# Performance work log

Hardware: AMD Instinct MI355X
Metric: run time of the kernel (lower is better)

Reference implementation:

```python
import jax, jax.numpy as jnp
import numpy as np

B, DIM, HID, K, G, MID = 1024, 384, 64, 8, 48, 128
EPS = 1e-06


def _gaussian_8x8():
    t = jnp.arange(K, dtype=jnp.float32) - 3.5
    g = jnp.exp(-(t[:, None] ** 2 + t[None, :] ** 2) / (2.0 * 2.0 ** 2))
    return g / g.sum()


def setup_inputs() -> dict:
    key = jax.random.key(0)
    ks = jax.random.split(key, 16)
    inp = {
        "x": jax.random.normal(ks[0], (B, DIM), dtype=jnp.float32),
        "W": jax.random.normal(ks[1], (DIM, HID), dtype=jnp.float32) * 0.02,
        "b": jax.random.normal(ks[2], (DIM, HID), dtype=jnp.float32) * 0.02,
        "patch_weight": _gaussian_8x8(),  # learnable 8x8, softmaxed in forward
        "pair_w1": jax.random.normal(ks[3], (G, G), dtype=jnp.float32) * 0.02,
        "pair_b1": jax.random.normal(ks[4], (G, G), dtype=jnp.float32) * 0.02,
        "pair_w2": jax.random.normal(ks[5], (G, G), dtype=jnp.float32) * 0.02,
        "pair_b2": jax.random.normal(ks[6], (G, G), dtype=jnp.float32) * 0.02,
        # nn.Linear(G, DIM)
        "proj_w": jax.random.normal(ks[7], (DIM, G), dtype=jnp.float32) * (1.0 / np.sqrt(G)),
        "proj_b": jax.random.normal(ks[8], (DIM,), dtype=jnp.float32) * 0.02,
        # nn.Linear(HID, MID)
        "down_w": jax.random.normal(ks[9], (MID, HID), dtype=jnp.float32) * (1.0 / np.sqrt(HID)),
        "down_b": jax.random.normal(ks[10], (MID,), dtype=jnp.float32) * 0.02,
        # nn.Linear(MID, HID)
        "up_w": jax.random.normal(ks[11], (HID, MID), dtype=jnp.float32) * (1.0 / np.sqrt(MID)),
        "up_b": jax.random.normal(ks[12], (HID,), dtype=jnp.float32) * 0.02,
    }
    return inp


def _leaky(v):
    return jnp.where(v >= 0, v, 0.01 * v)


def reference(x, W, b, patch_weight, pair_w1, pair_b1, pair_w2, pair_b2,
              proj_w, proj_b, down_w, down_b, up_w, up_b):
    # scale / inverse-bias GELU features: (B, DIM, HID)
    s = x[:, :, None]
    inv = 1.0 / (jnp.abs(s) + EPS)
    H = jax.nn.gelu(s * W[None] + inv * b[None], approximate=False)
    # Gram matrix over hidden dim: (B, DIM, DIM)
    P = jnp.einsum('bik,bjk->bij', H, H)
    # learnable gaussian patch pooling (softmax over flattened 8x8 weights)
    w = jax.nn.softmax(patch_weight.reshape(-1)).reshape(K, K)
    Pg = jnp.einsum('bgkhl,kl->bgh', P.reshape(-1, G, K, G, K), w)  # (B, G, G)
    # two elementwise gated leaky layers
    Pg = _leaky(Pg * pair_w1[None] + pair_b1[None])
    Pg = _leaky(Pg * pair_w2[None] + pair_b2[None])
    # softmax + nonlinear row reduction -> (B, G)
    row_soft = jax.nn.softmax(Pg, axis=-1)
    row_weights = (1.0 / (1.0 + row_soft ** 2)).sum(axis=-1)
    # project 48 -> 384, scale rows of H
    scales = row_weights @ proj_w.T + proj_b  # (B, DIM)
    H = H * scales[:, :, None]
    # tiny MLP on hidden dim
    z = _leaky(H @ down_w.T + down_b)
    z = _leaky(z @ up_w.T + up_b)
    return z
```

## Files before the change

### kernel.cpp

```cpp
#include <hip/hip_runtime.h>


#define EPSF 1e-6f

typedef __attribute__((ext_vector_type(8))) short bf16x8;
typedef __attribute__((ext_vector_type(4))) float f32x4;
typedef __attribute__((ext_vector_type(4))) unsigned short u16x4;

__device__ __forceinline__ unsigned short f2bf(float f) {
    union { float f; unsigned int u; } v; v.f = f;
    unsigned int r = v.u + 0x7fffu + ((v.u >> 16) & 1u);
    return (unsigned short)(r >> 16);
}
__device__ __forceinline__ float bf2f(unsigned short h) {
    union { unsigned int u; float f; } v; v.u = ((unsigned int)h) << 16;
    return v.f;
}
__device__ __forceinline__ float leaky(float v) { return v >= 0.0f ? v : 0.01f * v; }
__device__ __forceinline__ int key8(int r) { return (r ^ (r >> 3)) & 7; }
__device__ __forceinline__ float gelu_f(float u) {
    float t  = 0.7978845608028654f * (u + 0.044715f * u * u * u);
    float e  = __expf(2.0f * t);
    float th = 1.0f - 2.0f / (e + 1.0f);
    return 0.5f * u * (1.0f + th);
}

__global__ void prep(const float* __restrict__ proj_w,
                     const float* __restrict__ down_w,
                     const float* __restrict__ up_w,
                     float* __restrict__ ws) {
    int idx = blockIdx.x * blockDim.x + threadIdx.x;
    unsigned short* wb = (unsigned short*)(ws + 18432);
    if (idx < 18432) {
        int i = idx / 48, g = idx % 48;
        ws[g * 384 + i] = proj_w[idx];
    } else if (idx < 26624) {
        int k = idx - 18432;
        wb[k] = f2bf(down_w[k]);
    } else if (idx < 34816) {
        int k = idx - 26624;
        wb[8192 + k] = f2bf(up_w[k]);
    }
}

__global__ __launch_bounds__(512, 2) void fused_main(
    const float* __restrict__ x,
    const float* __restrict__ W,
    const float* __restrict__ bb,
    const float* __restrict__ patch_weight,
    const float* __restrict__ pw1, const float* __restrict__ pb1,
    const float* __restrict__ pw2, const float* __restrict__ pb2,
    const float* __restrict__ proj_b,
    const float* __restrict__ down_b,
    const float* __restrict__ up_b,
    const float* __restrict__ ws,
    float* __restrict__ out)
{
    __shared__ __align__(16) unsigned short sH[24576];
    __shared__ __align__(16) unsigned short sM[24576];
    __shared__ __align__(16) unsigned short sZ1[16384];
    __shared__ float sPg[48 * 49];
    __shared__ float sw[64];
    __shared__ float srw[48];
    __shared__ float sScale[384];
    __shared__ float sDb[128];
    __shared__ float sUb[64];

    const int t = threadIdx.x;
    const int b = blockIdx.x;
    const int wv = t >> 6, lane = t & 63, q = lane >> 4, r = lane & 15;
    const float* projT = ws;
    const unsigned short* dwB = (const unsigned short*)(ws + 18432);
    const unsigned short* uwB = dwB + 8192;
    unsigned short* sDW = sM;
    unsigned short* sUW = sM + 8192;

    if (t < 64) {
        float p = patch_weight[t];
        float m = p;
        for (int o = 32; o > 0; o >>= 1) m = fmaxf(m, __shfl_xor(m, o));
        float e = __expf(p - m);
        float s = e;
        for (int o = 32; o > 0; o >>= 1) s += __shfl_xor(s, o);
        sw[t] = e / s;
    }

    for (int j = 0; j < 12; ++j) {
        int idx4 = j * 512 + t;
        int base = idx4 * 4;
        int i = base >> 6, c0 = base & 63;
        float4 w4 = ((const float4*)W)[idx4];
        float4 b4 = ((const float4*)bb)[idx4];
        float xi  = x[b * 384 + i];
        float inv = 1.0f / (fabsf(xi) + EPSF);
        u16x4 hv;
        hv[0] = f2bf(gelu_f(xi * w4.x + inv * b4.x));
        hv[1] = f2bf(gelu_f(xi * w4.y + inv * b4.y));
        hv[2] = f2bf(gelu_f(xi * w4.z + inv * b4.z));
        hv[3] = f2bf(gelu_f(xi * w4.w + inv * b4.w));
        int cb = c0 >> 3, cc = c0 & 7;
        *(u16x4*)&sH[i * 64 + (cb ^ key8(i)) * 8 + cc] = hv;
    }
    __syncthreads();

    for (int jj = 0; jj < 6; ++jj) {
        int n = jj * 512 + t;
        int g = n >> 6, rem = n & 63, l = rem >> 3, cb = rem & 7;
        float acc[8];
        #pragma unroll
        for (int z = 0; z < 8; ++z) acc[z] = 0.0f;
        #pragma unroll
        for (int k = 0; k < 8; ++k) {
            int i = g * 8 + k;
            bf16x8 hv = *(const bf16x8*)&sH[i * 64 + (cb ^ key8(i)) * 8];
            float wk = sw[k * 8 + l];
            #pragma unroll
            for (int z = 0; z < 8; ++z) acc[z] += wk * bf2f((unsigned short)hv[z]);
        }
        int cbg = l * 8 + cb;
        int cbs = (cbg & ~7) | ((cbg ^ key8(g)) & 7);
        bf16x8 mv;
        #pragma unroll
        for (int z = 0; z < 8; ++z) mv[z] = (short)f2bf(acc[z]);
        *(bf16x8*)&sM[g * 512 + cbs * 8] = mv;
    }
    __syncthreads();

    for (int tt = wv; tt < 9; tt += 8) {
        int tg = tt / 3, th = tt % 3;
        f32x4 acc = {0.f, 0.f, 0.f, 0.f};
        for (int ks = 0; ks < 16; ++ks) {
            int kf = ks * 32 + q * 8;
            int g = tg * 16 + r;
            int cbg = kf >> 3;
            int cbs = (cbg & ~7) | ((cbg ^ key8(g)) & 7);
            bf16x8 av = *(const bf16x8*)&sM[g * 512 + cbs * 8];
            int h = th * 16 + r;
            int i = h * 8 + (kf >> 6);
            int cbh = (kf & 63) >> 3;
            bf16x8 bv = *(const bf16x8*)&sH[i * 64 + (cbh ^ key8(i)) * 8];
            acc = __builtin_amdgcn_mfma_f32_16x16x32_bf16(av, bv, acc, 0, 0, 0);
        }
        #pragma unroll
        for (int reg = 0; reg < 4; ++reg) {
            int g = tg * 16 + q * 4 + reg;
            int h = th * 16 + r;
            int idx = g * 48 + h;
            float v = acc[reg];
            v = leaky(v * pw1[idx] + pb1[idx]);
            v = leaky(v * pw2[idx] + pb2[idx]);
            sPg[g * 49 + h] = v;
        }
    }
    __syncthreads();

    if (t < 48) {
        const float* row = &sPg[t * 49];
        float mx = row[0];
        for (int h = 1; h < 48; ++h) mx = fmaxf(mx, row[h]);
        float s = 0.0f;
        for (int h = 0; h < 48; ++h) s += __expf(row[h] - mx);
        float invs = 1.0f / s;
        float rw = 0.0f;
        for (int h = 0; h < 48; ++h) {
            float p = __expf(row[h] - mx) * invs;
            rw += 1.0f / (1.0f + p * p);
        }
        srw[t] = rw;
    } else if (t >= 64) {
        for (int cid = t - 64; cid < 2048; cid += 448) {
            if (cid < 1024) {
                int nrow = cid >> 3, cb = cid & 7;
                bf16x8 v = *(const bf16x8*)&dwB[cid * 8];
                *(bf16x8*)&sDW[nrow * 64 + (cb ^ key8(nrow)) * 8] = v;
            } else {
                int c2 = cid - 1024;
                int rrow = c2 >> 4, cb = c2 & 15;
                bf16x8 v = *(const bf16x8*)&uwB[c2 * 8];
                int cbs = (cb & 8) | ((cb ^ key8(rrow)) & 7);
                *(bf16x8*)&sUW[rrow * 128 + cbs * 8] = v;
            }
        }
    }
    if (t >= 64 && t < 192)  sDb[t - 64]  = down_b[t - 64];
    if (t >= 192 && t < 256) sUb[t - 192] = up_b[t - 192];
    __syncthreads();

    if (t < 384) {
        float s = proj_b[t];
        for (int g = 0; g < 48; ++g) s += srw[g] * projT[g * 384 + t];
        sScale[t] = s;
    }
    __syncthreads();

    for (int rt = 0; rt < 3; ++rt) {
        {
            const int mt = wv;
            f32x4 acc[8];
            #pragma unroll
            for (int nt = 0; nt < 8; ++nt) acc[nt] = (f32x4){0.f, 0.f, 0.f, 0.f};
            #pragma unroll
            for (int ks = 0; ks < 2; ++ks) {
                int i = rt * 128 + mt * 16 + r;
                int cb = ks * 4 + q;
                bf16x8 av = *(const bf16x8*)&sH[i * 64 + (cb ^ key8(i)) * 8];
                #pragma unroll
                for (int nt = 0; nt < 8; ++nt) {
                    int nrow = nt * 16 + r;
                    bf16x8 bv = *(const bf16x8*)&sDW[nrow * 64 + (cb ^ key8(nrow)) * 8];
                    acc[nt] = __builtin_amdgcn_mfma_f32_16x16x32_bf16(av, bv, acc[nt], 0, 0, 0);
                }
            }
            #pragma unroll
            for (int nt = 0; nt < 8; ++nt) {
                #pragma unroll
                for (int reg = 0; reg < 4; ++reg) {
                    int rl = mt * 16 + q * 4 + reg;
                    int i = rt * 128 + rl;
                    int mm = nt * 16 + r;
                    float v = leaky(acc[nt][reg] * sScale[i] + sDb[mm]);
                    int cb = mm >> 3;
                    int cbs = (cb & 8) | ((cb ^ key8(rl)) & 7);
                    sZ1[rl * 128 + cbs * 8 + (mm & 7)] = f2bf(v);
                }
            }
        }
        __syncthreads();
        {
            const int mt = wv;
            f32x4 acc2[4];
            #pragma unroll
            for (int nt = 0; nt < 4; ++nt) acc2[nt] = (f32x4){0.f, 0.f, 0.f, 0.f};
            #pragma unroll
            for (int ks = 0; ks < 4; ++ks) {
                int rl = mt * 16 + r;
                int cb = ks * 4 + q;
                int cbs = (cb & 8) | ((cb ^ key8(rl)) & 7);
                bf16x8 av = *(const bf16x8*)&sZ1[rl * 128 + cbs * 8];
                #pragma unroll
                for (int nt = 0; nt < 4; ++nt) {
                    int nrow = nt * 16 + r;
                    int cbs2 = (cb & 8) | ((cb ^ key8(nrow)) & 7);
                    bf16x8 bv = *(const bf16x8*)&sUW[nrow * 128 + cbs2 * 8];
                    acc2[nt] = __builtin_amdgcn_mfma_f32_16x16x32_bf16(av, bv, acc2[nt], 0, 0, 0);
                }
            }
            #pragma unroll
            for (int nt = 0; nt < 4; ++nt) {
                #pragma unroll
                for (int reg = 0; reg < 4; ++reg) {
                    int i = rt * 128 + mt * 16 + q * 4 + reg;
                    int cp = nt * 16 + r;
                    float v = leaky(acc2[nt][reg] + sUb[cp]);
                    out[(b * 384 + i) * 64 + cp] = v;
                }
            }
        }
        __syncthreads();
    }
}

extern "C" void kernel_launch(void* const* d_in, const int* in_sizes, int n_in,
                              void* d_out, int out_size, void* d_ws, size_t ws_size,
                              hipStream_t stream) {
    const float* x      = (const float*)d_in[0];
    const float* W      = (const float*)d_in[1];
    const float* bb     = (const float*)d_in[2];
    const float* pw     = (const float*)d_in[3];
    const float* pw1    = (const float*)d_in[4];
    const float* pb1    = (const float*)d_in[5];
    const float* pw2    = (const float*)d_in[6];
    const float* pb2    = (const float*)d_in[7];
    const float* proj_w = (const float*)d_in[8];
    const float* proj_b = (const float*)d_in[9];
    const float* down_w = (const float*)d_in[10];
    const float* down_b = (const float*)d_in[11];
    const float* up_w   = (const float*)d_in[12];
    const float* up_b   = (const float*)d_in[13];
    float* out = (float*)d_out;
    float* ws  = (float*)d_ws;

    prep<<<(34816 + 255) / 256, 256, 0, stream>>>(proj_w, down_w, up_w, ws);
    fused_main<<<1024, 512, 0, stream>>>(x, W, bb, pw, pw1, pb1, pw2, pb2,
                                         proj_b, down_b, up_b, ws, out);
}
```

Before: 220.0 us.

## Use 1024-thread blocks, reshape MLP tiling, warp-parallel softmax, cheaper GELU math

Doubles the block size to 1024 threads and reworks every stage to match. Pooling now lets each thread produce four patch columns, and the per-row softmax becomes a wavefront shuffle reduction instead of a 48-thread serial loop. The MLP tiles change to 2 passes of 192 rows with a 4x4 wave grid, and shared buffers are aliased to fit. GELU, reciprocal and leaky are rewritten with rcp, fma and fmax. The intent is to cut serial phases and instruction count, at the cost of register pressure under __launch_bounds__(1024,4) and a larger LDS footprint that may limit occupancy.

Result: faster. 197.6 us (-10.2%).

```diff
diff --git a/kernel.cpp b/kernel.cpp
--- a/kernel.cpp
+++ b/kernel.cpp
@@ -16,13 +16,13 @@
     union { unsigned int u; float f; } v; v.u = ((unsigned int)h) << 16;
     return v.f;
 }
-__device__ __forceinline__ float leaky(float v) { return v >= 0.0f ? v : 0.01f * v; }
+__device__ __forceinline__ float leaky(float v) { return fmaxf(v, 0.01f * v); }
 __device__ __forceinline__ int key8(int r) { return (r ^ (r >> 3)) & 7; }
 __device__ __forceinline__ float gelu_f(float u) {
-    float t  = 0.7978845608028654f * (u + 0.044715f * u * u * u);
-    float e  = __expf(2.0f * t);
-    float th = 1.0f - 2.0f / (e + 1.0f);
-    return 0.5f * u * (1.0f + th);
+    float t = u * (1.5957691216f + 0.0713548163f * (u * u));
+    float e = __expf(t);
+    float r = __builtin_amdgcn_rcpf(e + 1.0f);
+    return fmaf(-u, r, u);
 }
 
 __global__ void prep(const float* __restrict__ proj_w,
@@ -43,7 +43,7 @@
     }
 }
 
-__global__ __launch_bounds__(512, 2) void fused_main(
+__global__ __launch_bounds__(1024, 4) void fused_main(
     const float* __restrict__ x,
     const float* __restrict__ W,
     const float* __restrict__ bb,
@@ -57,9 +57,8 @@
     float* __restrict__ out)
 {
     __shared__ __align__(16) unsigned short sH[24576];
-    __shared__ __align__(16) unsigned short sM[24576];
-    __shared__ __align__(16) unsigned short sZ1[16384];
-    __shared__ float sPg[48 * 49];
+    __shared__ __align__(16) unsigned short sRB[24576];
+    __shared__ __align__(16) unsigned short sZ1[24576];
     __shared__ float sw[64];
     __shared__ float srw[48];
     __shared__ float sScale[384];
@@ -72,8 +71,10 @@
     const float* projT = ws;
     const unsigned short* dwB = (const unsigned short*)(ws + 18432);
     const unsigned short* uwB = dwB + 8192;
-    unsigned short* sDW = sM;
-    unsigned short* sUW = sM + 8192;
+    unsigned short* sM  = sRB;
+    unsigned short* sDW = sRB;
+    unsigned short* sUW = sRB + 8192;
+    float* sPg = (float*)(sRB + 16384);
 
     if (t < 64) {
         float p = patch_weight[t];
@@ -82,177 +83,208 @@
         float e = __expf(p - m);
         float s = e;
         for (int o = 32; o > 0; o >>= 1) s += __shfl_xor(s, o);
-        sw[t] = e / s;
-    }
-
-    for (int j = 0; j < 12; ++j) {
-        int idx4 = j * 512 + t;
+        sw[t] = e * __builtin_amdgcn_rcpf(s);
+    }
+
+    for (int j = 0; j < 6; ++j) {
+        int idx4 = j * 1024 + t;
         int base = idx4 * 4;
         int i = base >> 6, c0 = base & 63;
         float4 w4 = ((const float4*)W)[idx4];
         float4 b4 = ((const float4*)bb)[idx4];
         float xi  = x[b * 384 + i];
-        float inv = 1.0f / (fabsf(xi) + EPSF);
+        float inv = __builtin_amdgcn_rcpf(fabsf(xi) + EPSF);
         u16x4 hv;
-        hv[0] = f2bf(gelu_f(xi * w4.x + inv * b4.x));
-        hv[1] = f2bf(gelu_f(xi * w4.y + inv * b4.y));
-        hv[2] = f2bf(gelu_f(xi * w4.z + inv * b4.z));
-        hv[3] = f2bf(gelu_f(xi * w4.w + inv * b4.w));
+        hv[0] = f2bf(gelu_f(fmaf(xi, w4.x, inv * b4.x)));
+        hv[1] = f2bf(gelu_f(fmaf(xi, w4.y, inv * b4.y)));
+        hv[2] = f2bf(gelu_f(fmaf(xi, w4.z, inv * b4.z)));
+        hv[3] = f2bf(gelu_f(fmaf(xi, w4.w, inv * b4.w)));
         int cb = c0 >> 3, cc = c0 & 7;
-        *(u16x4*)&sH[i * 64 + (cb ^ key8(i)) * 8 + cc] = hv;
-    }
-    __syncthreads();
-
-    for (int jj = 0; jj < 6; ++jj) {
-        int n = jj * 512 + t;
-        int g = n >> 6, rem = n & 63, l = rem >> 3, cb = rem & 7;
-        float acc[8];
-        #pragma unroll
-        for (int z = 0; z < 8; ++z) acc[z] = 0.0f;
+        *(u16x4*)&sH[i * 64 + ((cb ^ key8(i)) << 3) + cc] = hv;
+    }
+    __syncthreads();
+
+    if (t < 768) {
+        const int cb = t & 7, lq = (t >> 3) & 1, g = t >> 4;
+        float acc[4][8];
+        #pragma unroll
+        for (int a = 0; a < 4; ++a)
+            #pragma unroll
+            for (int cc = 0; cc < 8; ++cc) acc[a][cc] = 0.0f;
         #pragma unroll
         for (int k = 0; k < 8; ++k) {
             int i = g * 8 + k;
-            bf16x8 hv = *(const bf16x8*)&sH[i * 64 + (cb ^ key8(i)) * 8];
-            float wk = sw[k * 8 + l];
-            #pragma unroll
-            for (int z = 0; z < 8; ++z) acc[z] += wk * bf2f((unsigned short)hv[z]);
-        }
-        int cbg = l * 8 + cb;
-        int cbs = (cbg & ~7) | ((cbg ^ key8(g)) & 7);
-        bf16x8 mv;
-        #pragma unroll
-        for (int z = 0; z < 8; ++z) mv[z] = (short)f2bf(acc[z]);
-        *(bf16x8*)&sM[g * 512 + cbs * 8] = mv;
-    }
-    __syncthreads();
-
-    for (int tt = wv; tt < 9; tt += 8) {
-        int tg = tt / 3, th = tt % 3;
-        f32x4 acc = {0.f, 0.f, 0.f, 0.f};
+            bf16x8 hv = *(const bf16x8*)&sH[i * 64 + ((cb ^ key8(i)) << 3)];
+            f32x4 w4 = *(const f32x4*)&sw[k * 8 + lq * 4];
+            float hf[8];
+            #pragma unroll
+            for (int cc = 0; cc < 8; ++cc) hf[cc] = bf2f((unsigned short)hv[cc]);
+            #pragma unroll
+            for (int a = 0; a < 4; ++a)
+                #pragma unroll
+                for (int cc = 0; cc < 8; ++cc) acc[a][cc] = fmaf(w4[a], hf[cc], acc[a][cc]);
+        }
+        #pragma unroll
+        for (int a = 0; a < 4; ++a) {
+            int l = lq * 4 + a;
+            bf16x8 mv;
+            #pragma unroll
+            for (int cc = 0; cc < 8; ++cc) mv[cc] = (short)f2bf(acc[a][cc]);
+            *(bf16x8*)&sM[g * 512 + ((l * 8 + (cb ^ key8(g))) << 3)] = mv;
+        }
+    }
+    __syncthreads();
+
+    f32x4 pacc = {0.f, 0.f, 0.f, 0.f};
+    if (wv < 9) {
+        const int tg = wv / 3, th = wv % 3;
         for (int ks = 0; ks < 16; ++ks) {
             int kf = ks * 32 + q * 8;
             int g = tg * 16 + r;
             int cbg = kf >> 3;
             int cbs = (cbg & ~7) | ((cbg ^ key8(g)) & 7);
-            bf16x8 av = *(const bf16x8*)&sM[g * 512 + cbs * 8];
+            bf16x8 av = *(const bf16x8*)&sM[g * 512 + (cbs << 3)];
             int h = th * 16 + r;
             int i = h * 8 + (kf >> 6);
             int cbh = (kf & 63) >> 3;
-            bf16x8 bv = *(const bf16x8*)&sH[i * 64 + (cbh ^ key8(i)) * 8];
-            acc = __builtin_amdgcn_mfma_f32_16x16x32_bf16(av, bv, acc, 0, 0, 0);
+            bf16x8 bv = *(const bf16x8*)&sH[i * 64 + ((cbh ^ key8(i)) << 3)];
+            pacc = __builtin_amdgcn_mfma_f32_16x16x32_bf16(av, bv, pacc, 0, 0, 0);
         }
         #pragma unroll
         for (int reg = 0; reg < 4; ++reg) {
             int g = tg * 16 + q * 4 + reg;
             int h = th * 16 + r;
             int idx = g * 48 + h;
-            float v = acc[reg];
-            v = leaky(v * pw1[idx] + pb1[idx]);
-            v = leaky(v * pw2[idx] + pb2[idx]);
-            sPg[g * 49 + h] = v;
-        }
-    }
-    __syncthreads();
-
-    if (t < 48) {
-        const float* row = &sPg[t * 49];
-        float mx = row[0];
-        for (int h = 1; h < 48; ++h) mx = fmaxf(mx, row[h]);
-        float s = 0.0f;
-        for (int h = 0; h < 48; ++h) s += __expf(row[h] - mx);
-        float invs = 1.0f / s;
-        float rw = 0.0f;
-        for (int h = 0; h < 48; ++h) {
-            float p = __expf(row[h] - mx) * invs;
-            rw += 1.0f / (1.0f + p * p);
-        }
-        srw[t] = rw;
-    } else if (t >= 64) {
-        for (int cid = t - 64; cid < 2048; cid += 448) {
+            float v = pacc[reg];
+            v = leaky(fmaf(v, pw1[idx], pb1[idx]));
+            v = leaky(fmaf(v, pw2[idx], pb2[idx]));
+            pacc[reg] = v;
+        }
+    }
+    __syncthreads();
+
+    if (wv < 9) {
+        const int tg = wv / 3, th = wv % 3;
+        #pragma unroll
+        for (int reg = 0; reg < 4; ++reg) {
+            int g = tg * 16 + q * 4 + reg;
+            int h = th * 16 + r;
+            sPg[g * 49 + h] = pacc[reg];
+        }
+    } else {
+        for (int cid = t - 576; cid < 2048; cid += 448) {
             if (cid < 1024) {
                 int nrow = cid >> 3, cb = cid & 7;
                 bf16x8 v = *(const bf16x8*)&dwB[cid * 8];
-                *(bf16x8*)&sDW[nrow * 64 + (cb ^ key8(nrow)) * 8] = v;
+                *(bf16x8*)&sDW[nrow * 64 + ((cb ^ key8(nrow)) << 3)] = v;
             } else {
                 int c2 = cid - 1024;
                 int rrow = c2 >> 4, cb = c2 & 15;
                 bf16x8 v = *(const bf16x8*)&uwB[c2 * 8];
                 int cbs = (cb & 8) | ((cb ^ key8(rrow)) & 7);
-                *(bf16x8*)&sUW[rrow * 128 + cbs * 8] = v;
-            }
-        }
-    }
-    if (t >= 64 && t < 192)  sDb[t - 64]  = down_b[t - 64];
-    if (t >= 192 && t < 256) sUb[t - 192] = up_b[t - 192];
+                *(bf16x8*)&sUW[rrow * 128 + (cbs << 3)] = v;
+            }
+        }
+    }
+    if (t < 128) sDb[t] = down_b[t];
+    else if (t < 192) sUb[t - 128] = up_b[t - 128];
+    __syncthreads();
+
+    {
+        #pragma unroll
+        for (int rr = 0; rr < 3; ++rr) {
+            int row = wv + rr * 16;
+            float v = (lane < 48) ? sPg[row * 49 + lane] : -1e30f;
+            float m = v;
+            for (int o = 32; o > 0; o >>= 1) m = fmaxf(m, __shfl_xor(m, o));
+            float e = (lane < 48) ? __expf(v - m) : 0.0f;
+            float s = e;
+            for (int o = 32; o > 0; o >>= 1) s += __shfl_xor(s, o);
+            float p = e * __builtin_amdgcn_rcpf(s);
+            float rwv = (lane < 48) ? __builtin_amdgcn_rcpf(fmaf(p, p, 1.0f)) : 0.0f;
+            for (int o = 32; o > 0; o >>= 1) rwv += __shfl_xor(rwv, o);
+            if (lane == 0) srw[row] = rwv;
+        }
+    }
     __syncthreads();
 
     if (t < 384) {
         float s = proj_b[t];
-        for (int g = 0; g < 48; ++g) s += srw[g] * projT[g * 384 + t];
+        #pragma unroll 4
+        for (int g = 0; g < 48; ++g) s = fmaf(srw[g], projT[g * 384 + t], s);
         sScale[t] = s;
     }
     __syncthreads();
 
-    for (int rt = 0; rt < 3; ++rt) {
+    const int mg = wv >> 2, ng = wv & 3;
+    for (int rt = 0; rt < 2; ++rt) {
+        const int r0 = rt * 192;
         {
-            const int mt = wv;
-            f32x4 acc[8];
-            #pragma unroll
-            for (int nt = 0; nt < 8; ++nt) acc[nt] = (f32x4){0.f, 0.f, 0.f, 0.f};
+            f32x4 zacc[3][2];
+            #pragma unroll
+            for (int a = 0; a < 3; ++a)
+                #pragma unroll
+                for (int e = 0; e < 2; ++e) zacc[a][e] = (f32x4){0.f, 0.f, 0.f, 0.f};
             #pragma unroll
             for (int ks = 0; ks < 2; ++ks) {
-                int i = rt * 128 + mt * 16 + r;
                 int cb = ks * 4 + q;
-                bf16x8 av = *(const bf16x8*)&sH[i * 64 + (cb ^ key8(i)) * 8];
-                #pragma unroll
-                for (int nt = 0; nt < 8; ++nt) {
-                    int nrow = nt * 16 + r;
-                    bf16x8 bv = *(const bf16x8*)&sDW[nrow * 64 + (cb ^ key8(nrow)) * 8];
-                    acc[nt] = __builtin_amdgcn_mfma_f32_16x16x32_bf16(av, bv, acc[nt], 0, 0, 0);
-                }
-            }
-            #pragma unroll
-            for (int nt = 0; nt < 8; ++nt) {
-                #pragma unroll
-                for (int reg = 0; reg < 4; ++reg) {
-                    int rl = mt * 16 + q * 4 + reg;
-                    int i = rt * 128 + rl;
-                    int mm = nt * 16 + r;
-                    float v = leaky(acc[nt][reg] * sScale[i] + sDb[mm]);
-                    int cb = mm >> 3;
-                    int cbs = (cb & 8) | ((cb ^ key8(rl)) & 7);
-                    sZ1[rl * 128 + cbs * 8 + (mm & 7)] = f2bf(v);
+                bf16x8 af[3];
+                #pragma unroll
+                for (int a = 0; a < 3; ++a) {
+                    int i = r0 + (mg * 3 + a) * 16 + r;
+                    af[a] = *(const bf16x8*)&sH[i * 64 + ((cb ^ key8(i)) << 3)];
+                }
+                #pragma unroll
+                for (int e = 0; e < 2; ++e) {
+                    int n = (ng * 2 + e) * 16 + r;
+                    bf16x8 bv = *(const bf16x8*)&sDW[n * 64 + ((cb ^ key8(n)) << 3)];
+                    #pragma unroll
+                    for (int a = 0; a < 3; ++a)
+                        zacc[a][e] = __builtin_amdgcn_mfma_f32_16x16x32_bf16(af[a], bv, zacc[a][e], 0, 0, 0);
+                }
+            }
+            #pragma unroll
+            for (int a = 0; a < 3; ++a) {
+                #pragma unroll
+                for (int e = 0; e < 2; ++e) {
+                    #pragma unroll
+                    for (int reg = 0; reg < 4; ++reg) {
+                        int rl = (mg * 3 + a) * 16 + q * 4 + reg;
+                        int m = (ng * 2 + e) * 16 + r;
+                        float v = leaky(fmaf(zacc[a][e][reg], sScale[r0 + rl], sDb[m]));
+                        int cb2 = m >> 3;
+                        int cbs2 = (cb2 & 8) | ((cb2 ^ key8(rl)) & 7);
+                        sZ1[rl * 128 + (cbs2 << 3) + (m & 7)] = f2bf(v);
+                    }
                 }
             }
         }
         __syncthreads();
         {
-            const int mt = wv;
-            f32x4 acc2[4];
-            #pragma unroll
-            for (int nt = 0; nt < 4; ++nt) acc2[nt] = (f32x4){0.f, 0.f, 0.f, 0.f};
+            f32x4 oacc[3];
+            #pragma unroll
+            for (int a = 0; a < 3; ++a) oacc[a] = (f32x4){0.f, 0.f, 0.f, 0.f};
             #pragma unroll
             for (int ks = 0; ks < 4; ++ks) {
-                int rl = mt * 16 + r;
                 int cb = ks * 4 + q;
-                int cbs = (cb & 8) | ((cb ^ key8(rl)) & 7);
-                bf16x8 av = *(const bf16x8*)&sZ1[rl * 128 + cbs * 8];
-                #pragma unroll
-                for (int nt = 0; nt < 4; ++nt) {
-                    int nrow = nt * 16 + r;
-                    int cbs2 = (cb & 8) | ((cb ^ key8(nrow)) & 7);
-                    bf16x8 bv = *(const bf16x8*)&sUW[nrow * 128 + cbs2 * 8];
-                    acc2[nt] = __builtin_amdgcn_mfma_f32_16x16x32_bf16(av, bv, acc2[nt], 0, 0, 0);
-                }
-            }
-            #pragma unroll
-            for (int nt = 0; nt < 4; ++nt) {
+                int cp = ng * 16 + r;
+                int cbsB = (cb & 8) | ((cb ^ key8(cp)) & 7);
+                bf16x8 bv = *(const bf16x8*)&sUW[cp * 128 + (cbsB << 3)];
+                #pragma unroll
+                for (int a = 0; a < 3; ++a) {
+                    int rl = (mg * 3 + a) * 16 + r;
+                    int cbsA = (cb & 8) | ((cb ^ key8(rl)) & 7);
+                    bf16x8 av = *(const bf16x8*)&sZ1[rl * 128 + (cbsA << 3)];
+                    oacc[a] = __builtin_amdgcn_mfma_f32_16x16x32_bf16(av, bv, oacc[a], 0, 0, 0);
+                }
+            }
+            #pragma unroll
+            for (int a = 0; a < 3; ++a) {
                 #pragma unroll
                 for (int reg = 0; reg < 4; ++reg) {
-                    int i = rt * 128 + mt * 16 + q * 4 + reg;
-                    int cp = nt * 16 + r;
-                    float v = leaky(acc2[nt][reg] + sUb[cp]);
-                    out[(b * 384 + i) * 64 + cp] = v;
+                    int i = r0 + (mg * 3 + a) * 16 + q * 4 + reg;
+                    int cp = ng * 16 + r;
+                    out[(b * 384 + i) * 64 + cp] = leaky(oacc[a][reg] + sUb[cp]);
                 }
             }
         }
@@ -281,6 +313,6 @@
     float* ws  = (float*)d_ws;
 
     prep<<<(34816 + 255) / 256, 256, 0, stream>>>(proj_w, down_w, up_w, ws);
-    fused_main<<<1024, 512, 0, stream>>>(x, W, bb, pw, pw1, pb1, pw2, pb2,
-                                         proj_b, down_b, up_b, ws, out);
-}
+    fused_main<<<1024, 1024, 0, stream>>>(x, W, bb, pw, pw1, pb1, pw2, pb2,
+                                          proj_b, down_b, up_b, ws, out);
+}
```
